# Kernel tuning notes

Measured on AMD Instinct MI355X. Metric: run time of the kernel, lower is better.

Reference implementation:

```python
import jax, jax.numpy as jnp
import numpy as np

TEMPERATURE = 0.1
THRESHOLD = 0.2
EPS = 1e-12


def setup_inputs() -> dict:
    key = jax.random.key(0)
    k0, k1 = jax.random.split(key)
    f0 = jax.random.normal(k0, (1, 256, 80, 80), dtype=jnp.float32)
    f1 = jax.random.normal(k1, (1, 256, 80, 80), dtype=jnp.float32)
    return {"f0": f0, "f1": f1}


def reference(f0, f1):
    B, C, H0, W0 = f0.shape
    _, _, H1, W1 = f1.shape
    N0, N1 = H0 * W0, H1 * W1

    # (B, N, C), L2-normalized along C (matches F.normalize with eps clamp)
    f0_flat = f0.reshape(B, C, N0).transpose(0, 2, 1)
    f1_flat = f1.reshape(B, C, N1).transpose(0, 2, 1)
    f0n = f0_flat / jnp.maximum(jnp.linalg.norm(f0_flat, axis=-1, keepdims=True), EPS)
    f1n = f1_flat / jnp.maximum(jnp.linalg.norm(f1_flat, axis=-1, keepdims=True), EPS)

    # cosine similarity / temperature: (B, N0, N1)
    S = jnp.einsum('bnc,bmc->bnm', f0n, f1n) / TEMPERATURE
    # dual softmax
    P = jax.nn.softmax(S, axis=-1) * jax.nn.softmax(S, axis=-2)

    # mutual nearest-neighbor matching (B == 1 branch)
    conf = jnp.max(P[0], axis=-1)              # (N0,)
    indices0 = jnp.argmax(P[0], axis=-1)       # (N0,) row argmax
    indices1 = jnp.argmax(P[0], axis=-2)       # (N1,) column argmax
    ar0 = jnp.arange(N0)
    mutual = indices1[indices0] == ar0
    valid = mutual & (conf > THRESHOLD)        # (N0,) bool

    # fixed-shape (jit-friendly) match outputs: full grid, zeroed where invalid
    mkpts0 = jnp.stack([ar0 % W0, ar0 // W0], axis=1).astype(jnp.float32)
    mkpts1 = jnp.stack([indices0 % W1, indices0 // W1], axis=1).astype(jnp.float32)
    vf = valid[:, None].astype(jnp.float32)
    mkpts0 = mkpts0 * vf
    mkpts1 = mkpts1 * vf
    mconf = jnp.where(valid, conf, 0.0)

    return (P, mkpts0, mkpts1, mconf, valid)
```

## Files before the change

### kernel.cpp

```cpp
#include <hip/hip_runtime.h>

#define N0 6400
#define NC 256
#define WW 80

using half8   = __attribute__((ext_vector_type(8))) _Float16;
using floatx4 = __attribute__((ext_vector_type(4))) float;
#define GLOBAL_AS __attribute__((address_space(1)))
#define LDS_AS    __attribute__((address_space(3)))

__device__ __forceinline__ unsigned long long packvi(float v, int i) {
    return ((unsigned long long)__float_as_uint(v) << 32) | (unsigned int)i;
}

__global__ __launch_bounds__(256) void knorm(const float* __restrict__ f0,
                                             const float* __restrict__ f1,
                                             float* __restrict__ inv0,
                                             float* __restrict__ inv1) {
    int t = blockIdx.x * 256 + threadIdx.x;
    const float* src = (t < N0) ? f0 : f1;
    int n = (t < N0) ? t : (t - N0);
    float s = 0.f;
#pragma unroll 8
    for (int c = 0; c < NC; ++c) {
        float v = src[c * N0 + n];
        s += v * v;
    }
    float inv = 1.0f / fmaxf(sqrtf(s), 1e-12f);
    if (t < N0) inv0[n] = inv; else inv1[n] = inv;
}

__global__ __launch_bounds__(256) void ktrans(const float* __restrict__ src,
                                              const float* __restrict__ inv,
                                              _Float16* __restrict__ dst) {
    __shared__ float tile[32][33];
    int t = threadIdx.x;
    int n0 = blockIdx.x * 32, c0 = blockIdx.y * 32;
    int tx = t & 31, ty = t >> 5;
#pragma unroll
    for (int u = 0; u < 4; ++u)
        tile[ty + u * 8][tx] = src[(c0 + ty + u * 8) * N0 + n0 + tx];
    __syncthreads();
    int row = t >> 3;
    int cg  = (t & 7) * 4;
    int n = n0 + row;
    float iv = inv[n];
    union { ushort4 u4; _Float16 h[4]; } pk;
#pragma unroll
    for (int u = 0; u < 4; ++u)
        pk.h[u] = (_Float16)(tile[cg + u][row] * iv);
    *(ushort4*)&dst[n * NC + c0 + cg] = pk.u4;
}

__device__ __forceinline__ void gemm_core(const _Float16* __restrict__ A2,
                                          const _Float16* __restrict__ B2,
                                          unsigned short* ldsA, unsigned short* ldsB,
                                          int i0, int j0, int tid, int lane,
                                          int wm, int wn, floatx4 acc[4][4]) {
    int rl = tid >> 3;
    int cg = ((tid & 7) ^ (rl & 7)) * 8;
    int q  = lane >> 4;

    for (int k0 = 0; k0 < NC; k0 += 64) {
        __syncthreads();
#pragma unroll
        for (int g = 0; g < 4; ++g) {
            const _Float16* ga = A2 + (i0 + g * 32 + rl) * NC + k0 + cg;
            const _Float16* gb = B2 + (j0 + g * 32 + rl) * NC + k0 + cg;
            __builtin_amdgcn_global_load_lds((const GLOBAL_AS unsigned int*)ga,
                (LDS_AS unsigned int*)&ldsA[g * 2048 + tid * 8], 16, 0, 0);
            __builtin_amdgcn_global_load_lds((const GLOBAL_AS unsigned int*)gb,
                (LDS_AS unsigned int*)&ldsB[g * 2048 + tid * 8], 16, 0, 0);
        }
        __syncthreads();
#pragma unroll
        for (int s = 0; s < 2; ++s) {
            half8 af[4], bf[4];
#pragma unroll
            for (int mt = 0; mt < 4; ++mt) {
                int ra = wm * 64 + mt * 16 + (lane & 15);
                int ca = ((s * 4 + q) ^ (ra & 7)) * 8;
                af[mt] = *(const half8*)&ldsA[ra * 64 + ca];
                int rb = wn * 64 + mt * 16 + (lane & 15);
                int cb = ((s * 4 + q) ^ (rb & 7)) * 8;
                bf[mt] = *(const half8*)&ldsB[rb * 64 + cb];
            }
#pragma unroll
            for (int mt = 0; mt < 4; ++mt)
#pragma unroll
                for (int nt = 0; nt < 4; ++nt)
                    acc[mt][nt] = __builtin_amdgcn_mfma_f32_16x16x32_f16(
                        af[mt], bf[nt], acc[mt][nt], 0, 0, 0);
        }
    }
}

__global__ __launch_bounds__(256) void kgemm1(const _Float16* __restrict__ A2,
                                              const _Float16* __restrict__ B2,
                                              float* __restrict__ rowsum,
                                              float* __restrict__ colsum) {
    __shared__ __align__(16) unsigned short ldsA[8192], ldsB[8192];
    __shared__ float rs[128], cs[128];
    int tid = threadIdx.x, lane = tid & 63, wave = tid >> 6;
    int wm = wave & 1, wn = wave >> 1;
    int i0 = blockIdx.y * 128, j0 = blockIdx.x * 128;
    if (tid < 128) rs[tid] = 0.f; else cs[tid - 128] = 0.f;

    floatx4 acc[4][4] = {};
    gemm_core(A2, B2, ldsA, ldsB, i0, j0, tid, lane, wm, wn, acc);

    int quad = lane >> 4;
    float csum[4] = {0.f, 0.f, 0.f, 0.f};
#pragma unroll
    for (int mt = 0; mt < 4; ++mt)
#pragma unroll
        for (int r = 0; r < 4; ++r) {
            float rsv = 0.f;
#pragma unroll
            for (int nt = 0; nt < 4; ++nt) {
                float e = __expf(10.0f * acc[mt][nt][r]);
                rsv += e; csum[nt] += e;
            }
            rsv += __shfl_xor(rsv, 1);
            rsv += __shfl_xor(rsv, 2);
            rsv += __shfl_xor(rsv, 4);
            rsv += __shfl_xor(rsv, 8);
            if ((lane & 15) == 0) atomicAdd(&rs[wm * 64 + mt * 16 + quad * 4 + r], rsv);
        }
#pragma unroll
    for (int nt = 0; nt < 4; ++nt) {
        csum[nt] += __shfl_xor(csum[nt], 16);
        csum[nt] += __shfl_xor(csum[nt], 32);
    }
    if (lane < 16)
#pragma unroll
        for (int nt = 0; nt < 4; ++nt)
            atomicAdd(&cs[wn * 64 + nt * 16 + lane], csum[nt]);
    __syncthreads();
    if (tid < 128) atomicAdd(&rowsum[i0 + tid], rs[tid]);
    else           atomicAdd(&colsum[j0 + tid - 128], cs[tid - 128]);
}

__global__ __launch_bounds__(256) void kinv(float* __restrict__ sums) {
    int t = blockIdx.x * 256 + threadIdx.x;
    sums[t] = 1.0f / sums[t];
}

__global__ __launch_bounds__(256) void kgemm2(const _Float16* __restrict__ A2,
                                              const _Float16* __restrict__ B2,
                                              const float* __restrict__ invrow,
                                              const float* __restrict__ invcol,
                                              float* __restrict__ P,
                                              unsigned long long* __restrict__ rowbest,
                                              unsigned long long* __restrict__ colbest) {
    __shared__ __align__(16) unsigned short ldsA[8192], ldsB[8192];
    __shared__ unsigned long long rbst[128], cbst[128];
    int tid = threadIdx.x, lane = tid & 63, wave = tid >> 6;
    int wm = wave & 1, wn = wave >> 1;
    int i0 = blockIdx.y * 128, j0 = blockIdx.x * 128;
    if (tid < 128) rbst[tid] = 0ull; else cbst[tid - 128] = 0ull;

    floatx4 acc[4][4] = {};
    gemm_core(A2, B2, ldsA, ldsB, i0, j0, tid, lane, wm, wn, acc);

    int quad = lane >> 4;
    int cb0 = j0 + wn * 64 + (lane & 15);
    float invc[4];
#pragma unroll
    for (int nt = 0; nt < 4; ++nt) invc[nt] = invcol[cb0 + nt * 16];

    unsigned long long colb[4] = {0ull, 0ull, 0ull, 0ull};
#pragma unroll
    for (int mt = 0; mt < 4; ++mt) {
        int rb0 = i0 + wm * 64 + mt * 16 + quad * 4;
        float4 ir4 = *(const float4*)&invrow[rb0];
        float ir[4] = {ir4.x, ir4.y, ir4.z, ir4.w};
#pragma unroll
        for (int r = 0; r < 4; ++r) {
            int row = rb0 + r;
            unsigned long long rbv = 0ull;
#pragma unroll
            for (int nt = 0; nt < 4; ++nt) {
                float pv = __expf(20.0f * acc[mt][nt][r]) * ir[r] * invc[nt];
                P[row * N0 + cb0 + nt * 16] = pv;
                unsigned long long pr = packvi(pv, cb0 + nt * 16);
                if (pr > rbv) rbv = pr;
                unsigned long long pc = packvi(pv, row);
                if (pc > colb[nt]) colb[nt] = pc;
            }
#pragma unroll
            for (int s = 1; s < 16; s <<= 1) {
                unsigned long long o = __shfl_xor(rbv, s);
                if (o > rbv) rbv = o;
            }
            if ((lane & 15) == 0) atomicMax(&rbst[row - i0], rbv);
        }
    }
#pragma unroll
    for (int nt = 0; nt < 4; ++nt) {
        unsigned long long o = __shfl_xor(colb[nt], 16);
        if (o > colb[nt]) colb[nt] = o;
        o = __shfl_xor(colb[nt], 32);
        if (o > colb[nt]) colb[nt] = o;
    }
    if (lane < 16)
#pragma unroll
        for (int nt = 0; nt < 4; ++nt)
            atomicMax(&cbst[wn * 64 + nt * 16 + lane], colb[nt]);
    __syncthreads();
    if (tid < 128) atomicMax(&rowbest[i0 + tid], rbst[tid]);
    else           atomicMax(&colbest[j0 + tid - 128], cbst[tid - 128]);
}

__global__ __launch_bounds__(256) void kmatch(const unsigned long long* __restrict__ rowbest,
                                              const unsigned long long* __restrict__ colbest,
                                              float* __restrict__ out) {
    int i = blockIdx.x * 256 + threadIdx.x;
    unsigned long long rb = rowbest[i];
    float conf = __uint_as_float((unsigned int)(rb >> 32));
    int jj = (int)(rb & 0xffffffffu);
    unsigned long long cb = colbest[jj];
    int i2 = (int)(cb & 0xffffffffu);
    bool valid = (i2 == i) && (conf > 0.2f);
    float vf = valid ? 1.0f : 0.0f;

    float* mk0   = out + 40960000;
    float* mk1   = out + 40972800;
    float* mconf = out + 40985600;
    float* vout  = out + 40992000;
    mk0[i * 2 + 0] = vf * (float)(i % WW);
    mk0[i * 2 + 1] = vf * (float)(i / WW);
    mk1[i * 2 + 0] = vf * (float)(jj % WW);
    mk1[i * 2 + 1] = vf * (float)(jj / WW);
    mconf[i] = valid ? conf : 0.0f;
    vout[i]  = vf;
}

extern "C" void kernel_launch(void* const* d_in, const int* in_sizes, int n_in,
                              void* d_out, int out_size, void* d_ws, size_t ws_size,
                              hipStream_t stream) {
    const float* f0 = (const float*)d_in[0];
    const float* f1 = (const float*)d_in[1];
    float* out = (float*)d_out;

    _Float16* A2 = (_Float16*)d_ws;
    _Float16* B2 = A2 + 6400 * 256;
    float* inv0   = (float*)(B2 + 6400 * 256);
    float* inv1   = inv0 + 6400;
    float* rowsum = inv1 + 6400;
    float* colsum = rowsum + 6400;
    unsigned long long* rowbest = (unsigned long long*)(colsum + 6400);
    unsigned long long* colbest = rowbest + 6400;

    hipMemsetAsync(rowsum, 0, 153600, stream);

    knorm<<<50, 256, 0, stream>>>(f0, f1, inv0, inv1);
    ktrans<<<dim3(200, 8), 256, 0, stream>>>(f0, inv0, A2);
    ktrans<<<dim3(200, 8), 256, 0, stream>>>(f1, inv1, B2);
    kgemm1<<<dim3(50, 50), 256, 0, stream>>>(A2, B2, rowsum, colsum);
    kinv<<<50, 256, 0, stream>>>(rowsum);
    kgemm2<<<dim3(50, 50), 256, 0, stream>>>(A2, B2, rowsum, colsum,
                                             out, rowbest, colbest);
    kmatch<<<25, 256, 0, stream>>>(rowbest, colbest, out);
}
```

Measured before the change: 278.0 us.

## Stage full-K A panel in LDS and sweep ten B tiles per block

Both GEMM kernels now load the whole K=256 A row panel into LDS once. Each block then loops over ten 128-column B tiles, so only 250 blocks are launched instead of 2500. Row sums and row-best values stay in registers across tiles, and LDS atomics are replaced by direct global atomics per tile. The two transpose launches are merged and the inverse kernel is folded into kgemm2. The change gives up parallelism (250 blocks, one block per CU with 128KB LDS) and loses latency hiding between staging and MFMA, in exchange for less A reloading and fewer launches.

After: 275.1 us. About the same (-1.0%).

```diff
diff --git a/kernel.cpp b/kernel.cpp
--- a/kernel.cpp
+++ b/kernel.cpp
@@ -30,10 +30,16 @@
     if (t < N0) inv0[n] = inv; else inv1[n] = inv;
 }
 
-__global__ __launch_bounds__(256) void ktrans(const float* __restrict__ src,
-                                              const float* __restrict__ inv,
-                                              _Float16* __restrict__ dst) {
+__global__ __launch_bounds__(256) void ktrans(const float* __restrict__ f0,
+                                              const float* __restrict__ f1,
+                                              const float* __restrict__ inv0,
+                                              const float* __restrict__ inv1,
+                                              _Float16* __restrict__ A2,
+                                              _Float16* __restrict__ B2) {
     __shared__ float tile[32][33];
+    const float* src = blockIdx.z ? f1 : f0;
+    const float* inv = blockIdx.z ? inv1 : inv0;
+    _Float16* dst    = blockIdx.z ? B2 : A2;
     int t = threadIdx.x;
     int n0 = blockIdx.x * 32, c0 = blockIdx.y * 32;
     int tx = t & 31, ty = t >> 5;
@@ -52,164 +58,181 @@
     *(ushort4*)&dst[n * NC + c0 + cg] = pk.u4;
 }
 
-__device__ __forceinline__ void gemm_core(const _Float16* __restrict__ A2,
-                                          const _Float16* __restrict__ B2,
-                                          unsigned short* ldsA, unsigned short* ldsB,
-                                          int i0, int j0, int tid, int lane,
-                                          int wm, int wn, floatx4 acc[4][4]) {
+__device__ __forceinline__ void stage_panel(const _Float16* __restrict__ G,
+                                            unsigned short* lds, int r0, int tid) {
     int rl = tid >> 3;
-    int cg = ((tid & 7) ^ (rl & 7)) * 8;
-    int q  = lane >> 4;
-
-    for (int k0 = 0; k0 < NC; k0 += 64) {
-        __syncthreads();
+    int ch = ((tid & 7) ^ (rl & 7)) * 8;
+#pragma unroll
+    for (int kk = 0; kk < 4; ++kk)
 #pragma unroll
         for (int g = 0; g < 4; ++g) {
-            const _Float16* ga = A2 + (i0 + g * 32 + rl) * NC + k0 + cg;
-            const _Float16* gb = B2 + (j0 + g * 32 + rl) * NC + k0 + cg;
+            const _Float16* ga = G + (r0 + g * 32 + rl) * NC + kk * 64 + ch;
             __builtin_amdgcn_global_load_lds((const GLOBAL_AS unsigned int*)ga,
-                (LDS_AS unsigned int*)&ldsA[g * 2048 + tid * 8], 16, 0, 0);
-            __builtin_amdgcn_global_load_lds((const GLOBAL_AS unsigned int*)gb,
-                (LDS_AS unsigned int*)&ldsB[g * 2048 + tid * 8], 16, 0, 0);
-        }
-        __syncthreads();
-#pragma unroll
-        for (int s = 0; s < 2; ++s) {
-            half8 af[4], bf[4];
-#pragma unroll
-            for (int mt = 0; mt < 4; ++mt) {
-                int ra = wm * 64 + mt * 16 + (lane & 15);
-                int ca = ((s * 4 + q) ^ (ra & 7)) * 8;
-                af[mt] = *(const half8*)&ldsA[ra * 64 + ca];
-                int rb = wn * 64 + mt * 16 + (lane & 15);
-                int cb = ((s * 4 + q) ^ (rb & 7)) * 8;
-                bf[mt] = *(const half8*)&ldsB[rb * 64 + cb];
+                (LDS_AS unsigned int*)&lds[kk * 8192 + g * 2048 + tid * 8], 16, 0, 0);
+        }
+}
+
+__device__ __forceinline__ void tile_mfma(const unsigned short* ldsA,
+                                          const unsigned short* ldsB,
+                                          int lane, int wm, int wn,
+                                          floatx4 acc[4][4]) {
+    int q = lane >> 4;
+#pragma unroll
+    for (int s = 0; s < 8; ++s) {
+        int c  = s * 4 + q;
+        int kk = c >> 3, cq = c & 7;
+        half8 af[4], bf[4];
+#pragma unroll
+        for (int mt = 0; mt < 4; ++mt) {
+            int ra = wm * 64 + mt * 16 + (lane & 15);
+            af[mt] = *(const half8*)&ldsA[kk * 8192 + ra * 64 + ((cq ^ (ra & 7)) * 8)];
+            int rb = wn * 64 + mt * 16 + (lane & 15);
+            bf[mt] = *(const half8*)&ldsB[kk * 8192 + rb * 64 + ((cq ^ (rb & 7)) * 8)];
+        }
+#pragma unroll
+        for (int mt = 0; mt < 4; ++mt)
+#pragma unroll
+            for (int nt = 0; nt < 4; ++nt)
+                acc[mt][nt] = __builtin_amdgcn_mfma_f32_16x16x32_f16(
+                    af[mt], bf[nt], acc[mt][nt], 0, 0, 0);
+    }
+}
+
+__global__ __launch_bounds__(256, 1) void kgemm1(const _Float16* __restrict__ A2,
+                                                 const _Float16* __restrict__ B2,
+                                                 float* __restrict__ rowsum,
+                                                 float* __restrict__ colsum) {
+    __shared__ __align__(16) unsigned short ldsA[32768], ldsB[32768];
+    int tid = threadIdx.x, lane = tid & 63, wave = tid >> 6;
+    int wm = wave & 1, wn = wave >> 1, q = lane >> 4;
+    int i0 = blockIdx.x * 128, jp = blockIdx.y * 1280;
+
+    stage_panel(A2, ldsA, i0, tid);
+    float rsum[4][4] = {};
+
+    for (int jt = 0; jt < 10; ++jt) {
+        __syncthreads();
+        stage_panel(B2, ldsB, jp + jt * 128, tid);
+        __syncthreads();
+        floatx4 acc[4][4] = {};
+        tile_mfma(ldsA, ldsB, lane, wm, wn, acc);
+
+        float csum[4] = {0.f, 0.f, 0.f, 0.f};
+#pragma unroll
+        for (int mt = 0; mt < 4; ++mt)
+#pragma unroll
+            for (int r = 0; r < 4; ++r) {
+                float rv = 0.f;
+#pragma unroll
+                for (int nt = 0; nt < 4; ++nt) {
+                    float e = __expf(10.0f * acc[mt][nt][r]);
+                    rv += e; csum[nt] += e;
+                }
+                rsum[mt][r] += rv;
             }
 #pragma unroll
-            for (int mt = 0; mt < 4; ++mt)
-#pragma unroll
-                for (int nt = 0; nt < 4; ++nt)
-                    acc[mt][nt] = __builtin_amdgcn_mfma_f32_16x16x32_f16(
-                        af[mt], bf[nt], acc[mt][nt], 0, 0, 0);
-        }
-    }
-}
-
-__global__ __launch_bounds__(256) void kgemm1(const _Float16* __restrict__ A2,
-                                              const _Float16* __restrict__ B2,
-                                              float* __restrict__ rowsum,
-                                              float* __restrict__ colsum) {
-    __shared__ __align__(16) unsigned short ldsA[8192], ldsB[8192];
-    __shared__ float rs[128], cs[128];
+        for (int nt = 0; nt < 4; ++nt) {
+            csum[nt] += __shfl_xor(csum[nt], 16);
+            csum[nt] += __shfl_xor(csum[nt], 32);
+        }
+        if (lane < 16)
+#pragma unroll
+            for (int nt = 0; nt < 4; ++nt)
+                atomicAdd(&colsum[jp + jt * 128 + wn * 64 + nt * 16 + lane], csum[nt]);
+    }
+#pragma unroll
+    for (int mt = 0; mt < 4; ++mt)
+#pragma unroll
+        for (int r = 0; r < 4; ++r) {
+            float v = rsum[mt][r];
+            v += __shfl_xor(v, 1);
+            v += __shfl_xor(v, 2);
+            v += __shfl_xor(v, 4);
+            v += __shfl_xor(v, 8);
+            if ((lane & 15) == 0)
+                atomicAdd(&rowsum[i0 + wm * 64 + mt * 16 + q * 4 + r], v);
+        }
+}
+
+__global__ __launch_bounds__(256, 1) void kgemm2(const _Float16* __restrict__ A2,
+                                                 const _Float16* __restrict__ B2,
+                                                 const float* __restrict__ rowsum,
+                                                 const float* __restrict__ colsum,
+                                                 float* __restrict__ P,
+                                                 unsigned long long* __restrict__ rowbest,
+                                                 unsigned long long* __restrict__ colbest) {
+    __shared__ __align__(16) unsigned short ldsA[32768], ldsB[32768];
     int tid = threadIdx.x, lane = tid & 63, wave = tid >> 6;
-    int wm = wave & 1, wn = wave >> 1;
-    int i0 = blockIdx.y * 128, j0 = blockIdx.x * 128;
-    if (tid < 128) rs[tid] = 0.f; else cs[tid - 128] = 0.f;
-
-    floatx4 acc[4][4] = {};
-    gemm_core(A2, B2, ldsA, ldsB, i0, j0, tid, lane, wm, wn, acc);
-
-    int quad = lane >> 4;
-    float csum[4] = {0.f, 0.f, 0.f, 0.f};
+    int wm = wave & 1, wn = wave >> 1, q = lane >> 4;
+    int i0 = blockIdx.x * 128, jp = blockIdx.y * 1280;
+
+    stage_panel(A2, ldsA, i0, tid);
+
+    float ir[4][4];
+#pragma unroll
+    for (int mt = 0; mt < 4; ++mt) {
+        float4 v4 = *(const float4*)&rowsum[i0 + wm * 64 + mt * 16 + q * 4];
+        ir[mt][0] = 1.0f / v4.x; ir[mt][1] = 1.0f / v4.y;
+        ir[mt][2] = 1.0f / v4.z; ir[mt][3] = 1.0f / v4.w;
+    }
+
+    unsigned long long rbv[4][4] = {};
+
+    for (int jt = 0; jt < 10; ++jt) {
+        __syncthreads();
+        stage_panel(B2, ldsB, jp + jt * 128, tid);
+        __syncthreads();
+        floatx4 acc[4][4] = {};
+        tile_mfma(ldsA, ldsB, lane, wm, wn, acc);
+
+        int cb0 = jp + jt * 128 + wn * 64 + (lane & 15);
+        float ic[4];
+#pragma unroll
+        for (int nt = 0; nt < 4; ++nt) ic[nt] = 1.0f / colsum[cb0 + nt * 16];
+
+        unsigned long long colb[4] = {0ull, 0ull, 0ull, 0ull};
+#pragma unroll
+        for (int mt = 0; mt < 4; ++mt) {
+            int rb0 = i0 + wm * 64 + mt * 16 + q * 4;
+#pragma unroll
+            for (int r = 0; r < 4; ++r) {
+                int row = rb0 + r;
+#pragma unroll
+                for (int nt = 0; nt < 4; ++nt) {
+                    float pv = __expf(20.0f * acc[mt][nt][r]) * ir[mt][r] * ic[nt];
+                    P[row * N0 + cb0 + nt * 16] = pv;
+                    unsigned long long pr = packvi(pv, cb0 + nt * 16);
+                    if (pr > rbv[mt][r]) rbv[mt][r] = pr;
+                    unsigned long long pc = packvi(pv, row);
+                    if (pc > colb[nt]) colb[nt] = pc;
+                }
+            }
+        }
+#pragma unroll
+        for (int nt = 0; nt < 4; ++nt) {
+            unsigned long long o = __shfl_xor(colb[nt], 16);
+            if (o > colb[nt]) colb[nt] = o;
+            o = __shfl_xor(colb[nt], 32);
+            if (o > colb[nt]) colb[nt] = o;
+        }
+        if (lane < 16)
+#pragma unroll
+            for (int nt = 0; nt < 4; ++nt)
+                atomicMax(&colbest[cb0 + nt * 16], colb[nt]);
+    }
 #pragma unroll
     for (int mt = 0; mt < 4; ++mt)
 #pragma unroll
         for (int r = 0; r < 4; ++r) {
-            float rsv = 0.f;
-#pragma unroll
-            for (int nt = 0; nt < 4; ++nt) {
-                float e = __expf(10.0f * acc[mt][nt][r]);
-                rsv += e; csum[nt] += e;
+            unsigned long long v = rbv[mt][r];
+#pragma unroll
+            for (int s = 1; s < 16; s <<= 1) {
+                unsigned long long o = __shfl_xor(v, s);
+                if (o > v) v = o;
             }
-            rsv += __shfl_xor(rsv, 1);
-            rsv += __shfl_xor(rsv, 2);
-            rsv += __shfl_xor(rsv, 4);
-            rsv += __shfl_xor(rsv, 8);
-            if ((lane & 15) == 0) atomicAdd(&rs[wm * 64 + mt * 16 + quad * 4 + r], rsv);
-        }
-#pragma unroll
-    for (int nt = 0; nt < 4; ++nt) {
-        csum[nt] += __shfl_xor(csum[nt], 16);
-        csum[nt] += __shfl_xor(csum[nt], 32);
-    }
-    if (lane < 16)
-#pragma unroll
-        for (int nt = 0; nt < 4; ++nt)
-            atomicAdd(&cs[wn * 64 + nt * 16 + lane], csum[nt]);
-    __syncthreads();
-    if (tid < 128) atomicAdd(&rowsum[i0 + tid], rs[tid]);
-    else           atomicAdd(&colsum[j0 + tid - 128], cs[tid - 128]);
-}
-
-__global__ __launch_bounds__(256) void kinv(float* __restrict__ sums) {
-    int t = blockIdx.x * 256 + threadIdx.x;
-    sums[t] = 1.0f / sums[t];
-}
-
-__global__ __launch_bounds__(256) void kgemm2(const _Float16* __restrict__ A2,
-                                              const _Float16* __restrict__ B2,
-                                              const float* __restrict__ invrow,
-                                              const float* __restrict__ invcol,
-                                              float* __restrict__ P,
-                                              unsigned long long* __restrict__ rowbest,
-                                              unsigned long long* __restrict__ colbest) {
-    __shared__ __align__(16) unsigned short ldsA[8192], ldsB[8192];
-    __shared__ unsigned long long rbst[128], cbst[128];
-    int tid = threadIdx.x, lane = tid & 63, wave = tid >> 6;
-    int wm = wave & 1, wn = wave >> 1;
-    int i0 = blockIdx.y * 128, j0 = blockIdx.x * 128;
-    if (tid < 128) rbst[tid] = 0ull; else cbst[tid - 128] = 0ull;
-
-    floatx4 acc[4][4] = {};
-    gemm_core(A2, B2, ldsA, ldsB, i0, j0, tid, lane, wm, wn, acc);
-
-    int quad = lane >> 4;
-    int cb0 = j0 + wn * 64 + (lane & 15);
-    float invc[4];
-#pragma unroll
-    for (int nt = 0; nt < 4; ++nt) invc[nt] = invcol[cb0 + nt * 16];
-
-    unsigned long long colb[4] = {0ull, 0ull, 0ull, 0ull};
-#pragma unroll
-    for (int mt = 0; mt < 4; ++mt) {
-        int rb0 = i0 + wm * 64 + mt * 16 + quad * 4;
-        float4 ir4 = *(const float4*)&invrow[rb0];
-        float ir[4] = {ir4.x, ir4.y, ir4.z, ir4.w};
-#pragma unroll
-        for (int r = 0; r < 4; ++r) {
-            int row = rb0 + r;
-            unsigned long long rbv = 0ull;
-#pragma unroll
-            for (int nt = 0; nt < 4; ++nt) {
-                float pv = __expf(20.0f * acc[mt][nt][r]) * ir[r] * invc[nt];
-                P[row * N0 + cb0 + nt * 16] = pv;
-                unsigned long long pr = packvi(pv, cb0 + nt * 16);
-                if (pr > rbv) rbv = pr;
-                unsigned long long pc = packvi(pv, row);
-                if (pc > colb[nt]) colb[nt] = pc;
-            }
-#pragma unroll
-            for (int s = 1; s < 16; s <<= 1) {
-                unsigned long long o = __shfl_xor(rbv, s);
-                if (o > rbv) rbv = o;
-            }
-            if ((lane & 15) == 0) atomicMax(&rbst[row - i0], rbv);
-        }
-    }
-#pragma unroll
-    for (int nt = 0; nt < 4; ++nt) {
-        unsigned long long o = __shfl_xor(colb[nt], 16);
-        if (o > colb[nt]) colb[nt] = o;
-        o = __shfl_xor(colb[nt], 32);
-        if (o > colb[nt]) colb[nt] = o;
-    }
-    if (lane < 16)
-#pragma unroll
-        for (int nt = 0; nt < 4; ++nt)
-            atomicMax(&cbst[wn * 64 + nt * 16 + lane], colb[nt]);
-    __syncthreads();
-    if (tid < 128) atomicMax(&rowbest[i0 + tid], rbst[tid]);
-    else           atomicMax(&colbest[j0 + tid - 128], cbst[tid - 128]);
+            if ((lane & 15) == 0)
+                atomicMax(&rowbest[i0 + wm * 64 + mt * 16 + q * 4 + r], v);
+        }
 }
 
 __global__ __launch_bounds__(256) void kmatch(const unsigned long long* __restrict__ rowbest,
@@ -255,11 +278,9 @@
     hipMemsetAsync(rowsum, 0, 153600, stream);
 
     knorm<<<50, 256, 0, stream>>>(f0, f1, inv0, inv1);
-    ktrans<<<dim3(200, 8), 256, 0, stream>>>(f0, inv0, A2);
-    ktrans<<<dim3(200, 8), 256, 0, stream>>>(f1, inv1, B2);
-    kgemm1<<<dim3(50, 50), 256, 0, stream>>>(A2, B2, rowsum, colsum);
-    kinv<<<50, 256, 0, stream>>>(rowsum);
-    kgemm2<<<dim3(50, 50), 256, 0, stream>>>(A2, B2, rowsum, colsum,
-                                             out, rowbest, colbest);
+    ktrans<<<dim3(200, 8, 2), 256, 0, stream>>>(f0, f1, inv0, inv1, A2, B2);
+    kgemm1<<<dim3(50, 5), 256, 0, stream>>>(A2, B2, rowsum, colsum);
+    kgemm2<<<dim3(50, 5), 256, 0, stream>>>(A2, B2, rowsum, colsum,
+                                            out, rowbest, colbest);
     kmatch<<<25, 256, 0, stream>>>(rowbest, colbest, out);
 }
```
